# Kernel tuning notes

Hardware: AMD Instinct MI355X
Metric: run time of the kernel (lower is better)

## Reference

```python
import jax, jax.numpy as jnp
import numpy as np

B, T, DM, D, W, DG = 2, 4096, 2048, 4096, 4, 512  # batch, seq, model hidden, conv channels (value_dim), kernel size, generator hidden


def setup_inputs() -> dict:
    key = jax.random.key(0)
    k0, k1, k2, k3, k4 = jax.random.split(key, 5)
    return {
        "x": jax.random.normal(k0, (B, T, D), jnp.float32) * 0.02,
        "generator_input": jax.random.normal(k1, (B, T, DM), jnp.float32) * 0.02,
        "w1": jax.random.normal(k2, (DG, DM), jnp.float32) * 0.02,   # Linear(DM -> DG), no bias
        "w2": jax.random.normal(k3, (D * W, DG), jnp.float32) * 0.02,  # Linear(DG -> D*W)
        "b2": jax.random.normal(k4, (D * W,), jnp.float32) * 0.02,
    }


def reference(x, generator_input, w1, w2, b2):
    # Hypernetwork: per-token depthwise conv kernels [B, T, D, W]
    h = jax.nn.silu(jnp.einsum("btm,gm->btg", generator_input, w1))
    kflat = jnp.einsum("btg,kg->btk", h, w2) + b2
    kernels = kflat.reshape(x.shape[0], x.shape[1], x.shape[2], W)
    # Causal depthwise conv: left-pad by W-1, windowed multiply-accumulate.
    xp = jnp.pad(x, ((0, 0), (W - 1, 0), (0, 0)))
    Tlen = x.shape[1]
    y = kernels[..., 0] * xp[:, 0:Tlen, :]
    for w in range(1, W):
        y = y + kernels[..., w] * xp[:, w:w + Tlen, :]
    return jax.nn.silu(y)  # [B, T, D]
```

## Files before the change

### kernel.cpp

```cpp
#include <hip/hip_runtime.h>
#include <hip/hip_bf16.h>
#include <stdint.h>

#define TLEN 4096
#define DMm  2048
#define DD   4096
#define DGg  512
#define BT   8192
#define DW   16384

typedef __attribute__((ext_vector_type(8))) short bf16x8;
typedef __attribute__((ext_vector_type(4))) float f32x4;

__device__ __forceinline__ unsigned short f2bf(float f) {
    union { float f; unsigned u; } c; c.f = f;
    unsigned u = c.u;
    unsigned r = (u + 0x7FFFu + ((u >> 16) & 1u)) >> 16;
    return (unsigned short)r;
}

#define NB1 (BT * DMm / 4)
#define NB2 (DGg * DMm / 4)
#define NB3 (DW * DGg / 4)
__global__ void cast_all_kernel(const float* __restrict__ g,
                                const float* __restrict__ w1,
                                const float* __restrict__ w2,
                                unsigned short* __restrict__ o) {
    int i = blockIdx.x * blockDim.x + threadIdx.x;
    if (i >= NB1 + NB2 + NB3) return;
    const float* src; int j = i;
    if (j < NB1) { src = g; }
    else if (j < NB1 + NB2) { src = w1; j -= NB1; }
    else { src = w2; j -= NB1 + NB2; }
    float4 v = reinterpret_cast<const float4*>(src)[j];
    ushort4 u;
    u.x = f2bf(v.x); u.y = f2bf(v.y); u.z = f2bf(v.z); u.w = f2bf(v.w);
    reinterpret_cast<ushort4*>(o)[i] = u;
}

#define GLDS16(gp, lp)                                                         \
    __builtin_amdgcn_global_load_lds(                                          \
        (__attribute__((address_space(1))) const void*)(gp),                   \
        (__attribute__((address_space(3))) void*)(lp), 16, 0, 0)

#define VMCNT(n) asm volatile("s_waitcnt vmcnt(" #n ")" ::: "memory")
#define SBAR()   __builtin_amdgcn_s_barrier()
#define SCHED0() __builtin_amdgcn_sched_barrier(0)

#define G1_B 12288

__global__ __launch_bounds__(256, 2) void gemm1_silu_kernel(
    const unsigned short* __restrict__ Gen_b,
    const unsigned short* __restrict__ W1b,
    unsigned short* __restrict__ H)
{
    __shared__ __attribute__((aligned(16))) char lds[36864];
    const int tid  = threadIdx.x;
    const int lane = tid & 63, wave = tid >> 6;
    const int wm   = wave >> 1, wn = wave & 1;
    const int la   = lane & 15, hi = lane >> 4;

    int bid = blockIdx.x;
    int swz = (bid & 7) * 64 + (bid >> 3);
    const int g0 = (swz & 7) * 64;
    const int t0 = (swz >> 3) * 128;

    const int srow = lane >> 2;
    const int scol = ((lane & 3) ^ ((srow >> 1) & 3)) * 8;

    auto stageA = [&](int tk, int p) {
        int row = wave * 16 + srow;
        GLDS16(W1b + (size_t)(g0 + row) * DMm + tk * 32 + scol,
               lds + p * 4096 + wave * 1024);
    };
    auto stageB = [&](int tk, int p) {
#pragma unroll
        for (int q = 0; q < 2; ++q) {
            int chunk = wave * 2 + q, row = chunk * 16 + srow;
            GLDS16(Gen_b + (size_t)(t0 + row) * DMm + tk * 32 + scol,
                   lds + G1_B + p * 8192 + chunk * 1024);
        }
    };

    f32x4 acc[2][4] = {};
    const int slotb = (hi ^ ((la >> 1) & 3)) * 16;
    const int aOff  = (wm * 32 + la) * 64 + slotb;
    const int bOff  = G1_B + (wn * 64 + la) * 64 + slotb;

    auto region = [&](int r, bool doStage) {
        const int p = r % 3;
        const char* aB = lds + p * 4096 + aOff;
        const char* bB = lds + p * 8192 + bOff;
        bf16x8 aF[2], bF[4];
#pragma unroll
        for (int m = 0; m < 2; ++m)
            aF[m] = *reinterpret_cast<const bf16x8*>(aB + m * 1024);
#pragma unroll
        for (int nr = 0; nr < 4; ++nr)
            bF[nr] = *reinterpret_cast<const bf16x8*>(bB + nr * 1024);
        if (doStage) { stageA(r + 2, (r + 2) % 3); stageB(r + 2, (r + 2) % 3); }
        SCHED0();
        __builtin_amdgcn_s_setprio(1);
#pragma unroll
        for (int m = 0; m < 2; ++m)
#pragma unroll
            for (int nr = 0; nr < 4; ++nr)
                acc[m][nr] = __builtin_amdgcn_mfma_f32_16x16x32_bf16(
                    aF[m], bF[nr], acc[m][nr], 0, 0, 0);
        __builtin_amdgcn_s_setprio(0);
        SCHED0();
    };

    stageA(0, 0); stageB(0, 0);
    stageA(1, 1); stageB(1, 1);
    VMCNT(3);
    SBAR();

    for (int r = 0; r < 62; ++r) {
        region(r, true);
        VMCNT(3);
        SBAR();
    }
    region(62, false); VMCNT(0); SBAR();
    region(63, false);

    __syncthreads();

    unsigned short* smY = reinterpret_cast<unsigned short*>(lds);
#pragma unroll
    for (int nr = 0; nr < 4; ++nr) {
        int tl = wn * 64 + nr * 16 + la;
#pragma unroll
        for (int m = 0; m < 2; ++m) {
            int gl0 = wm * 32 + m * 16 + hi * 4;
#pragma unroll
            for (int j = 0; j < 4; ++j) {
                float v = acc[m][nr][j];
                smY[tl * 72 + gl0 + j] = f2bf(v / (1.0f + __expf(-v)));
            }
        }
    }
    __syncthreads();

    for (int c = tid; c < 128 * 8; c += 256) {
        int row = c >> 3, q = c & 7;
        bf16x8 v = *reinterpret_cast<const bf16x8*>(&smY[row * 72 + q * 8]);
        *reinterpret_cast<bf16x8*>(&H[(size_t)(t0 + row) * DGg + g0 + q * 8]) = v;
    }
}

#define LDS_B2 49152

__global__ __launch_bounds__(512, 4) void gemm2_conv_silu_kernel(
    const unsigned short* __restrict__ Hb,
    const unsigned short* __restrict__ W2b,
    const float* __restrict__ b2,
    const float* __restrict__ x,
    float* __restrict__ out)
{
    __shared__ __attribute__((aligned(16))) char lds[73728];
    const int tid  = threadIdx.x;
    const int lane = tid & 63, wave = tid >> 6;
    const int wm   = wave >> 1, wn = wave & 1;
    const int la   = lane & 15, hi = lane >> 4;

    int bid = blockIdx.x;
    int swz = (bid & 7) * 512 + (bid >> 3);
    const int n0 = (swz >> 6) * 256;
    const int t0 = (swz & 63) * 128;
    const int d0 = n0 >> 2;

    const int srow = lane >> 2;
    const int scol = ((lane & 3) ^ ((srow >> 1) & 3)) * 8;

    auto stageA = [&](int tk, int p) {
#pragma unroll
        for (int q = 0; q < 2; ++q) {
            int chunk = wave * 2 + q, row = chunk * 16 + srow;
            GLDS16(W2b + (size_t)(n0 + row) * DGg + tk * 32 + scol,
                   lds + p * 16384 + chunk * 1024);
        }
    };
    auto stageB = [&](int tk, int p) {
        int row = wave * 16 + srow;
        GLDS16(Hb + (size_t)(t0 + row) * DGg + tk * 32 + scol,
               lds + LDS_B2 + p * 8192 + wave * 1024);
    };

    f32x4 acc[4][4] = {};
    const int slotb = (hi ^ ((la >> 1) & 3)) * 16;
    const int aOff  = (wm * 64 + la) * 64 + slotb;
    const int bOff  = LDS_B2 + (wn * 64 + la) * 64 + slotb;

    auto region = [&](int r, bool doStage) {
        const int p = r % 3;
        const char* aB = lds + p * 16384 + aOff;
        const char* bB = lds + p * 8192 + bOff;
        bf16x8 aF[4], bF[4];
#pragma unroll
        for (int m = 0; m < 4; ++m)
            aF[m] = *reinterpret_cast<const bf16x8*>(aB + m * 1024);
#pragma unroll
        for (int nr = 0; nr < 4; ++nr)
            bF[nr] = *reinterpret_cast<const bf16x8*>(bB + nr * 1024);
        if (doStage) { stageA(r + 2, (r + 2) % 3); stageB(r + 2, (r + 2) % 3); }
        SCHED0();
        __builtin_amdgcn_s_setprio(1);
#pragma unroll
        for (int m = 0; m < 4; ++m)
#pragma unroll
            for (int nr = 0; nr < 4; ++nr)
                acc[m][nr] = __builtin_amdgcn_mfma_f32_16x16x32_bf16(
                    aF[m], bF[nr], acc[m][nr], 0, 0, 0);
        __builtin_amdgcn_s_setprio(0);
        SCHED0();
    };

    stageA(0, 0); stageB(0, 0);
    stageA(1, 1); stageB(1, 1);
    VMCNT(3);
    SBAR();

#pragma unroll
    for (int r = 0; r < 14; ++r) {
        region(r, true);
        VMCNT(3);
        SBAR();
    }
    region(14, false); VMCNT(0); SBAR();
    region(15, false);

    float4 xv[5];
#pragma unroll
    for (int k = 0; k < 5; ++k) {
        int c = tid + k * 512;
        float4 v = make_float4(0.f, 0.f, 0.f, 0.f);
        if (c < 2096) {
            int row = c >> 4, q = c & 15;
            int rg = t0 - 3 + row;
            if (rg >= 0 && (rg >> 12) == (t0 >> 12))
                v = *reinterpret_cast<const float4*>(&x[(size_t)rg * DD + d0 + q * 4]);
        }
        xv[k] = v;
    }
    __syncthreads();

    float* smX = reinterpret_cast<float*>(lds);
#pragma unroll
    for (int k = 0; k < 5; ++k) {
        int c = tid + k * 512;
        if (c < 2096) {
            int row = c >> 4, q = c & 15;
            *reinterpret_cast<float4*>(&smX[row * 68 + q * 4]) = xv[k];
        }
    }
    __syncthreads();

    float4 bb[4];
#pragma unroll
    for (int m = 0; m < 4; ++m)
        bb[m] = *reinterpret_cast<const float4*>(&b2[n0 + wm * 64 + m * 16 + hi * 4]);

    float* smY = reinterpret_cast<float*>(lds + 35632);
#pragma unroll
    for (int nr = 0; nr < 4; ++nr) {
        int tl = wn * 64 + nr * 16 + la;
#pragma unroll
        for (int m = 0; m < 4; ++m) {
            int dl = wm * 16 + m * 4 + hi;
            float pv =
                  (acc[m][nr][0] + bb[m].x) * smX[(tl + 0) * 68 + dl]
                + (acc[m][nr][1] + bb[m].y) * smX[(tl + 1) * 68 + dl]
                + (acc[m][nr][2] + bb[m].z) * smX[(tl + 2) * 68 + dl]
                + (acc[m][nr][3] + bb[m].w) * smX[(tl + 3) * 68 + dl];
            smY[tl * 68 + dl] = pv / (1.0f + __expf(-pv));
        }
    }
    __syncthreads();

    for (int c = tid; c < 128 * 16; c += 512) {
        int row = c >> 4, q = c & 15;
        float4 v = *reinterpret_cast<const float4*>(&smY[row * 68 + q * 4]);
        *reinterpret_cast<float4*>(&out[(size_t)(t0 + row) * DD + d0 + q * 4]) = v;
    }
}

extern "C" void kernel_launch(void* const* d_in, const int* in_sizes, int n_in,
                              void* d_out, int out_size, void* d_ws, size_t ws_size,
                              hipStream_t stream) {
    const float* x   = (const float*)d_in[0];
    const float* gen = (const float*)d_in[1];
    const float* w1  = (const float*)d_in[2];
    const float* w2  = (const float*)d_in[3];
    const float* b2  = (const float*)d_in[4];
    float* out = (float*)d_out;

    char* ws = (char*)d_ws;
    size_t off = 0;
    unsigned short* gen_b = (unsigned short*)(ws + off); off += (size_t)BT * DMm * 2;
    unsigned short* w1_b  = (unsigned short*)(ws + off); off += (size_t)DGg * DMm * 2;
    unsigned short* w2_b  = (unsigned short*)(ws + off); off += (size_t)DW * DGg * 2;
    unsigned short* h_b   = (unsigned short*)(ws + off); off += (size_t)BT * DGg * 2;

    int total4 = NB1 + NB2 + NB3;
    cast_all_kernel<<<(total4 + 255) / 256, 256, 0, stream>>>(gen, w1, w2, gen_b);

    gemm1_silu_kernel<<<512, 256, 0, stream>>>(gen_b, w1_b, h_b);
    gemm2_conv_silu_kernel<<<4096, 512, 0, stream>>>(h_b, w2_b, b2, x, out);
}
```

Baseline: 232.8 us.

## Fuse fp32-to-bf16 cast of gen and w1 into GEMM1 register-staged pipeline

```diff
diff --git a/kernel.cpp b/kernel.cpp
--- a/kernel.cpp
+++ b/kernel.cpp
@@ -18,21 +18,17 @@
     unsigned r = (u + 0x7FFFu + ((u >> 16) & 1u)) >> 16;
     return (unsigned short)r;
 }
-
-#define NB1 (BT * DMm / 4)
-#define NB2 (DGg * DMm / 4)
+__device__ __forceinline__ unsigned short f2bf_n(float f) {
+    __hip_bfloat16 h = __float2bfloat16(f);
+    return *reinterpret_cast<unsigned short*>(&h);
+}
+
 #define NB3 (DW * DGg / 4)
-__global__ void cast_all_kernel(const float* __restrict__ g,
-                                const float* __restrict__ w1,
-                                const float* __restrict__ w2,
-                                unsigned short* __restrict__ o) {
+__global__ void cast_w2_kernel(const float* __restrict__ w2,
+                               unsigned short* __restrict__ o) {
     int i = blockIdx.x * blockDim.x + threadIdx.x;
-    if (i >= NB1 + NB2 + NB3) return;
-    const float* src; int j = i;
-    if (j < NB1) { src = g; }
-    else if (j < NB1 + NB2) { src = w1; j -= NB1; }
-    else { src = w2; j -= NB1 + NB2; }
-    float4 v = reinterpret_cast<const float4*>(src)[j];
+    if (i >= NB3) return;
+    float4 v = reinterpret_cast<const float4*>(w2)[i];
     ushort4 u;
     u.x = f2bf(v.x); u.y = f2bf(v.y); u.z = f2bf(v.z); u.w = f2bf(v.w);
     reinterpret_cast<ushort4*>(o)[i] = u;
@@ -44,14 +40,15 @@
         (__attribute__((address_space(3))) void*)(lp), 16, 0, 0)
 
 #define VMCNT(n) asm volatile("s_waitcnt vmcnt(" #n ")" ::: "memory")
+#define LGKM0()  asm volatile("s_waitcnt lgkmcnt(0)" ::: "memory")
 #define SBAR()   __builtin_amdgcn_s_barrier()
 #define SCHED0() __builtin_amdgcn_sched_barrier(0)
 
 #define G1_B 12288
 
 __global__ __launch_bounds__(256, 2) void gemm1_silu_kernel(
-    const unsigned short* __restrict__ Gen_b,
-    const unsigned short* __restrict__ W1b,
+    const float* __restrict__ gen,
+    const float* __restrict__ w1,
     unsigned short* __restrict__ H)
 {
     __shared__ __attribute__((aligned(16))) char lds[36864];
@@ -65,21 +62,35 @@
     const int g0 = (swz & 7) * 64;
     const int t0 = (swz >> 3) * 128;
 
-    const int srow = lane >> 2;
-    const int scol = ((lane & 3) ^ ((srow >> 1) & 3)) * 8;
-
-    auto stageA = [&](int tk, int p) {
-        int row = wave * 16 + srow;
-        GLDS16(W1b + (size_t)(g0 + row) * DMm + tk * 32 + scol,
-               lds + p * 4096 + wave * 1024);
-    };
-    auto stageB = [&](int tk, int p) {
-#pragma unroll
-        for (int q = 0; q < 2; ++q) {
-            int chunk = wave * 2 + q, row = chunk * 16 + srow;
-            GLDS16(Gen_b + (size_t)(t0 + row) * DMm + tk * 32 + scol,
-                   lds + G1_B + p * 8192 + chunk * 1024);
-        }
+    const int arow = tid >> 2, aslot = tid & 3;
+    const int brow = tid >> 2;
+
+    auto issue = [&](float4 (&A)[2], float4 (&B0)[2], float4 (&B1)[2], int tk) {
+        const float* pa = w1 + (size_t)(g0 + arow) * DMm + tk * 32 + aslot * 8;
+        A[0] = *reinterpret_cast<const float4*>(pa);
+        A[1] = *reinterpret_cast<const float4*>(pa + 4);
+        const float* pb0 = gen + (size_t)(t0 + brow) * DMm + tk * 32 + aslot * 8;
+        B0[0] = *reinterpret_cast<const float4*>(pb0);
+        B0[1] = *reinterpret_cast<const float4*>(pb0 + 4);
+        const float* pb1 = gen + (size_t)(t0 + 64 + brow) * DMm + tk * 32 + aslot * 8;
+        B1[0] = *reinterpret_cast<const float4*>(pb1);
+        B1[1] = *reinterpret_cast<const float4*>(pb1 + 4);
+    };
+    auto packStore = [&](char* dst, const float4& v0, const float4& v1) {
+        union { bf16x8 v; unsigned short s[8]; } u;
+        u.s[0] = f2bf_n(v0.x); u.s[1] = f2bf_n(v0.y);
+        u.s[2] = f2bf_n(v0.z); u.s[3] = f2bf_n(v0.w);
+        u.s[4] = f2bf_n(v1.x); u.s[5] = f2bf_n(v1.y);
+        u.s[6] = f2bf_n(v1.z); u.s[7] = f2bf_n(v1.w);
+        *reinterpret_cast<bf16x8*>(dst) = u.v;
+    };
+    auto cvtWrite = [&](float4 (&A)[2], float4 (&B0)[2], float4 (&B1)[2], int p) {
+        packStore(lds + p * 4096 + arow * 64 + ((aslot ^ ((arow >> 1) & 3)) * 16),
+                  A[0], A[1]);
+        packStore(lds + G1_B + p * 8192 + brow * 64 +
+                      ((aslot ^ ((brow >> 1) & 3)) * 16), B0[0], B0[1]);
+        packStore(lds + G1_B + p * 8192 + (brow + 64) * 64 +
+                      ((aslot ^ (((brow + 64) >> 1) & 3)) * 16), B1[0], B1[1]);
     };
 
     f32x4 acc[2][4] = {};
@@ -87,7 +98,12 @@
     const int aOff  = (wm * 32 + la) * 64 + slotb;
     const int bOff  = G1_B + (wn * 64 + la) * 64 + slotb;
 
-    auto region = [&](int r, bool doStage) {
+    float4 sA0[2], sB00[2], sB01[2];
+    float4 sA1[2], sB10[2], sB11[2];
+
+    auto body = [&](int r, float4 (&IA)[2], float4 (&IB0)[2], float4 (&IB1)[2],
+                    float4 (&WA)[2], float4 (&WB0)[2], float4 (&WB1)[2],
+                    bool doIssue, bool doWrite, bool v6) {
         const int p = r % 3;
         const char* aB = lds + p * 4096 + aOff;
         const char* bB = lds + p * 8192 + bOff;
@@ -98,7 +114,7 @@
 #pragma unroll
         for (int nr = 0; nr < 4; ++nr)
             bF[nr] = *reinterpret_cast<const bf16x8*>(bB + nr * 1024);
-        if (doStage) { stageA(r + 2, (r + 2) % 3); stageB(r + 2, (r + 2) % 3); }
+        if (doIssue) issue(IA, IB0, IB1, r + 2);
         SCHED0();
         __builtin_amdgcn_s_setprio(1);
 #pragma unroll
@@ -109,20 +125,27 @@
                     aF[m], bF[nr], acc[m][nr], 0, 0, 0);
         __builtin_amdgcn_s_setprio(0);
         SCHED0();
-    };
-
-    stageA(0, 0); stageB(0, 0);
-    stageA(1, 1); stageB(1, 1);
-    VMCNT(3);
+        if (doWrite) {
+            if (v6) VMCNT(6); else VMCNT(0);
+            cvtWrite(WA, WB0, WB1, (r + 1) % 3);
+            LGKM0();
+            SBAR();
+        }
+    };
+
+    issue(sA0, sB00, sB01, 0);
+    issue(sA1, sB10, sB11, 1);
+    VMCNT(6);
+    cvtWrite(sA0, sB00, sB01, 0);
+    LGKM0();
     SBAR();
 
     for (int r = 0; r < 62; ++r) {
-        region(r, true);
-        VMCNT(3);
-        SBAR();
-    }
-    region(62, false); VMCNT(0); SBAR();
-    region(63, false);
+        if (r & 1) body(r, sA1, sB10, sB11, sA0, sB00, sB01, true, true, true);
+        else       body(r, sA0, sB00, sB01, sA1, sB10, sB11, true, true, true);
+    }
+    body(62, sA0, sB00, sB01, sA1, sB10, sB11, false, true, false);
+    body(63, sA0, sB00, sB01, sA1, sB10, sB11, false, false, false);
 
     __syncthreads();
 
@@ -216,20 +239,6 @@
         SCHED0();
     };
 
-    stageA(0, 0); stageB(0, 0);
-    stageA(1, 1); stageB(1, 1);
-    VMCNT(3);
-    SBAR();
-
-#pragma unroll
-    for (int r = 0; r < 14; ++r) {
-        region(r, true);
-        VMCNT(3);
-        SBAR();
-    }
-    region(14, false); VMCNT(0); SBAR();
-    region(15, false);
-
     float4 xv[5];
 #pragma unroll
     for (int k = 0; k < 5; ++k) {
@@ -243,6 +252,20 @@
         }
         xv[k] = v;
     }
+    stageA(0, 0); stageB(0, 0);
+    stageA(1, 1); stageB(1, 1);
+    VMCNT(3);
+    SBAR();
+
+#pragma unroll
+    for (int r = 0; r < 14; ++r) {
+        region(r, true);
+        VMCNT(3);
+        SBAR();
+    }
+    region(14, false); VMCNT(0); SBAR();
+    region(15, false);
+
     __syncthreads();
 
     float* smX = reinterpret_cast<float*>(lds);
@@ -297,14 +320,10 @@
 
     char* ws = (char*)d_ws;
     size_t off = 0;
-    unsigned short* gen_b = (unsigned short*)(ws + off); off += (size_t)BT * DMm * 2;
-    unsigned short* w1_b  = (unsigned short*)(ws + off); off += (size_t)DGg * DMm * 2;
-    unsigned short* w2_b  = (unsigned short*)(ws + off); off += (size_t)DW * DGg * 2;
-    unsigned short* h_b   = (unsigned short*)(ws + off); off += (size_t)BT * DGg * 2;
-
-    int total4 = NB1 + NB2 + NB3;
-    cast_all_kernel<<<(total4 + 255) / 256, 256, 0, stream>>>(gen, w1, w2, gen_b);
-
-    gemm1_silu_kernel<<<512, 256, 0, stream>>>(gen_b, w1_b, h_b);
+    unsigned short* w2_b = (unsigned short*)(ws + off); off += (size_t)DW * DGg * 2;
+    unsigned short* h_b  = (unsigned short*)(ws + off); off += (size_t)BT * DGg * 2;
+
+    cast_w2_kernel<<<(NB3 + 255) / 256, 256, 0, stream>>>(w2, w2_b);
+    gemm1_silu_kernel<<<512, 256, 0, stream>>>(gen, w1, h_b);
     gemm2_conv_silu_kernel<<<4096, 512, 0, stream>>>(h_b, w2_b, b2, x, out);
 }
```

New measurement: 275.5 us. 18.4% more time.
